# Optimization experiments

Measured on AMD Instinct MI355X. Metric: run time of the kernel, lower is better.

## Reference

```python
import jax, jax.numpy as jnp
import numpy as np

NUM_NODES = 100000
NUM_EDGES = 1600000
NUM_GRAPHS = 64
IN_CH, HID, NCLS = 15, 128, 11


def setup_inputs() -> dict:
    key = jax.random.key(0)
    ks = jax.random.split(key, 9)
    x = jax.random.normal(ks[0], (NUM_NODES, IN_CH), dtype=jnp.float32)
    edge_index = jax.random.randint(ks[1], (2, NUM_EDGES), 0, NUM_NODES, dtype=jnp.int64)
    batch = jnp.sort(jax.random.randint(ks[2], (NUM_NODES,), 0, NUM_GRAPHS, dtype=jnp.int64))
    s1 = 1.0 / np.sqrt(IN_CH)
    s2 = 1.0 / np.sqrt(HID)
    W1 = jax.random.normal(ks[3], (IN_CH, HID), dtype=jnp.float32) * s1
    b1 = jax.random.normal(ks[4], (HID,), dtype=jnp.float32) * s1
    W2 = jax.random.normal(ks[5], (HID, HID), dtype=jnp.float32) * s2
    b2 = jax.random.normal(ks[6], (HID,), dtype=jnp.float32) * s2
    Wf = jax.random.normal(ks[7], (HID, NCLS), dtype=jnp.float32) * s2
    bf = jax.random.normal(ks[8], (NCLS,), dtype=jnp.float32) * s2
    return {"x": x, "edge_index": edge_index, "batch": batch,
            "W1": W1, "b1": b1, "W2": W2, "b2": b2, "Wf": Wf, "bf": bf}


def reference(x, edge_index, batch, W1, b1, W2, b2, Wf, bf):
    N = x.shape[0]
    loop = jnp.arange(N, dtype=edge_index.dtype)
    # PyG GCNConv: add self-loops, symmetric D^{-1/2} A D^{-1/2} normalization
    src = jnp.concatenate([edge_index[0], loop])
    dst = jnp.concatenate([edge_index[1], loop])
    deg = jax.ops.segment_sum(jnp.ones(src.shape[0], dtype=x.dtype), dst, num_segments=N)
    dinv = deg ** -0.5  # deg >= 1 due to self-loops
    norm = (dinv[src] * dinv[dst])[:, None]  # [E+N, 1]

    def gcn(h, W, b):
        m = h @ W                                   # transform first (smaller gather)
        agg = jax.ops.segment_sum(m[src] * norm, dst, num_segments=N)
        return agg + b

    h = jax.nn.relu(gcn(x, W1, b1))
    h = jax.nn.relu(gcn(h, W2, b2))

    # global_mean_pool over graph ids
    sums = jax.ops.segment_sum(h, batch, num_segments=NUM_GRAPHS)
    cnts = jax.ops.segment_sum(jnp.ones((N,), dtype=h.dtype), batch, num_segments=NUM_GRAPHS)
    pooled = sums / jnp.maximum(cnts, 1.0)[:, None]  # [G, HID]
    return pooled @ Wf + bf                          # [G, NCLS]
```

## Files before the change

kernel.cpp:

```cpp
#include <hip/hip_runtime.h>

#define N_NODES 100000
#define N_EDGES 1600000
#define N_GRAPHS 64
#define IN_CH 15
#define HID 128
#define NCLS 11

#define NBUCK 196
#define NBF 512
#define EPB (N_EDGES / NBF)

using short8 = __attribute__((ext_vector_type(8))) short;
using f32x4 = __attribute__((ext_vector_type(4))) float;
using f32x2 = __attribute__((ext_vector_type(2))) float;

__device__ __forceinline__ unsigned short f2bf(float f) {
    unsigned u = __builtin_bit_cast(unsigned, f);
    u += 0x7FFF + ((u >> 16) & 1);
    return (unsigned short)(u >> 16);
}
__device__ __forceinline__ unsigned packbf(float a, float b) {
    return (unsigned)f2bf(a) | ((unsigned)f2bf(b) << 16);
}
__device__ __forceinline__ float2 unpackbf(unsigned v) {
    float2 r;
    unsigned lo = v << 16;
    unsigned hi = v & 0xFFFF0000u;
    r.x = __builtin_bit_cast(float, lo);
    r.y = __builtin_bit_cast(float, hi);
    return r;
}

__device__ __forceinline__ unsigned char f2fp8(float f) {
    return (unsigned char)(__builtin_amdgcn_cvt_pk_fp8_f32(f, f, 0, false) & 0xFF);
}
__device__ __forceinline__ float2 unpackfp8(unsigned short v) {
    f32x2 r = __builtin_amdgcn_cvt_pk_f32_fp8((int)(unsigned)v, false);
    return make_float2(r[0], r[1]);
}

__global__ __launch_bounds__(256) void k_init(float* __restrict__ pooled) {
    int i = blockIdx.x * 256 + threadIdx.x;
    if (i < N_GRAPHS * HID) pooled[i] = 0.f;
}

__global__ __launch_bounds__(256) void k_hist(const int* __restrict__ dst,
                                              int* __restrict__ cntm) {
    __shared__ int hist[NBUCK];
    int t = threadIdx.x;
    for (int i = t; i < NBUCK; i += 256) hist[i] = 0;
    __syncthreads();
    int base = blockIdx.x * EPB;
#pragma unroll
    for (int i = 0; i < (EPB + 255) / 256; ++i) {
        int e = i * 256 + t;
        if (e < EPB) atomicAdd(&hist[dst[base + e] >> 9], 1);
    }
    __syncthreads();
    for (int b = t; b < NBUCK; b += 256)
        cntm[b * NBF + blockIdx.x] = hist[b];
}

__global__ __launch_bounds__(256) void k_btot(const int* __restrict__ cntm,
                                              int* __restrict__ tot) {
    __shared__ int red[256];
    int b = blockIdx.x, t = threadIdx.x;
    red[t] = cntm[b * NBF + t] + cntm[b * NBF + t + 256];
    __syncthreads();
    for (int off = 128; off > 0; off >>= 1) {
        if (t < off) red[t] += red[t + off];
        __syncthreads();
    }
    if (t == 0) tot[b] = red[0];
}

__global__ __launch_bounds__(256) void k_bscan(const int* __restrict__ tot,
                                               int* __restrict__ bbase,
                                               int* __restrict__ rowptr) {
    __shared__ int arr[256];
    int t = threadIdx.x;
    arr[t] = (t < NBUCK) ? tot[t] : 0;
    __syncthreads();
    for (int off = 1; off < 256; off <<= 1) {
        int v = (t >= off) ? arr[t - off] : 0;
        __syncthreads();
        arr[t] += v;
        __syncthreads();
    }
    if (t < NBUCK) bbase[t] = (t == 0) ? 0 : arr[t - 1];
    if (t == 0) rowptr[N_NODES] = N_EDGES;
}

__global__ __launch_bounds__(NBF) void k_offs(const int* __restrict__ cntm,
                                              const int* __restrict__ bbase,
                                              int* __restrict__ offs) {
    __shared__ int arr[NBF];
    int b = blockIdx.x, t = threadIdx.x;
    arr[t] = cntm[b * NBF + t];
    __syncthreads();
    for (int off = 1; off < NBF; off <<= 1) {
        int v = (t >= off) ? arr[t - off] : 0;
        __syncthreads();
        arr[t] += v;
        __syncthreads();
    }
    offs[b * NBF + t] = bbase[b] + ((t == 0) ? 0 : arr[t - 1]);
}

__global__ __launch_bounds__(256) void k_partition(const int* __restrict__ src,
                                                   const int* __restrict__ dst,
                                                   const int* __restrict__ offs,
                                                   unsigned* __restrict__ staging) {
    __shared__ int cur[NBUCK];
    int t = threadIdx.x;
    for (int b = t; b < NBUCK; b += 256) cur[b] = offs[b * NBF + blockIdx.x];
    __syncthreads();
    int base = blockIdx.x * EPB;
#pragma unroll
    for (int i = 0; i < (EPB + 255) / 256; ++i) {
        int e = i * 256 + t;
        if (e < EPB) {
            int d = dst[base + e];
            int s = src[base + e];
            int slot = atomicAdd(&cur[d >> 9], 1);
            staging[slot] = ((unsigned)(d & 511) << 17) | (unsigned)s;
        }
    }
}

__global__ __launch_bounds__(256) void k_fuse(const unsigned* __restrict__ staging,
                                              const int* __restrict__ bbase,
                                              int* __restrict__ rowptr,
                                              float* __restrict__ dinv,
                                              int* __restrict__ csr_src) {
    __shared__ int cnt[512];
    __shared__ int cur[512];
    __shared__ int arr[256];
    int b = blockIdx.x, t = threadIdx.x;
    cnt[t] = 0; cnt[t + 256] = 0;
    __syncthreads();
    int beg = bbase[b];
    int end = (b == NBUCK - 1) ? N_EDGES : bbase[b + 1];
    for (int e = beg + t; e < end; e += 256)
        atomicAdd(&cnt[staging[e] >> 17], 1);
    __syncthreads();
    int c0 = cnt[2 * t], c1 = cnt[2 * t + 1];
    arr[t] = c0 + c1;
    __syncthreads();
    for (int off = 1; off < 256; off <<= 1) {
        int v = (t >= off) ? arr[t - off] : 0;
        __syncthreads();
        arr[t] += v;
        __syncthreads();
    }
    int excl = (t == 0) ? 0 : arr[t - 1];
    int p0 = beg + excl;
    int p1 = p0 + c0;
    cur[2 * t] = p0;
    cur[2 * t + 1] = p1;
    int n0 = b << 9;
    int n = n0 + 2 * t;
    if (n < N_NODES) { rowptr[n] = p0; dinv[n] = rsqrtf((float)(c0 + 1)); }
    n = n0 + 2 * t + 1;
    if (n < N_NODES) { rowptr[n] = p1; dinv[n] = rsqrtf((float)(c1 + 1)); }
    __syncthreads();
    for (int e = beg + t; e < end; e += 256) {
        unsigned v = staging[e];
        int pos = atomicAdd(&cur[v >> 17], 1);
        csr_src[pos] = (int)(v & 0x1FFFFu);
    }
}

__global__ __launch_bounds__(256) void k_w2pack(const float* __restrict__ W2,
                                                uint4* __restrict__ Bp) {
    int i = blockIdx.x * 256 + threadIdx.x;
    if (i >= 2048) return;
    int lane = i & 63;
    int kb = (i >> 6) & 3;
    int ct = i >> 8;
    int col = ct * 16 + (lane & 15);
    int k0 = kb * 32 + ((lane >> 4) & 3) * 8;
    unsigned w[4];
#pragma unroll
    for (int p = 0; p < 4; ++p) {
        int k = k0 + 2 * p;
        w[p] = packbf(W2[k * HID + col], W2[(k + 1) * HID + col]);
    }
    Bp[i] = make_uint4(w[0], w[1], w[2], w[3]);
}

__global__ __launch_bounds__(256) void k_prescale(const float* __restrict__ x,
                                                  const float* __restrict__ dinv,
                                                  unsigned* __restrict__ xs) {
    int i = blockIdx.x * 256 + threadIdx.x;
    if (i >= N_NODES * 8) return;
    int n = i >> 3, p = i & 7;
    float dv = dinv[n];
    int c0 = 2 * p, c1 = c0 + 1;
    float a = x[(size_t)n * IN_CH + c0] * dv;
    float b = (c1 < IN_CH) ? x[(size_t)n * IN_CH + c1] * dv : 0.f;
    xs[i] = packbf(a, b);
}

__global__ __launch_bounds__(256) void k_gather15(const int* __restrict__ rowptr,
                                                  const int* __restrict__ csr_src,
                                                  const unsigned* __restrict__ xs,
                                                  const float* __restrict__ dinv,
                                                  float* __restrict__ agg) {
    int wave = (blockIdx.x * 256 + threadIdx.x) >> 6;
    if (wave >= N_NODES) return;
    int n = wave;
    int l = threadIdx.x & 63;
    unsigned g = (unsigned)(l >> 3), cp = (unsigned)(l & 7);
    int beg = rowptr[n], end = rowptr[n + 1];
    float2 acc = make_float2(0.f, 0.f);
    for (int e = beg + (int)g; e < end; e += 8) {
        unsigned s = (unsigned)csr_src[e];
        float2 v = unpackbf(xs[s * 8u + cp]);
        acc.x += v.x; acc.y += v.y;
    }
#pragma unroll
    for (int off = 8; off < 64; off <<= 1) {
        acc.x += __shfl_xor(acc.x, off, 64);
        acc.y += __shfl_xor(acc.y, off, 64);
    }
    if (l < 8) {
        float2 s = unpackbf(xs[(unsigned)n * 8u + (unsigned)l]);
        float dv = dinv[n];
        float2 r = make_float2((acc.x + s.x) * dv, (acc.y + s.y) * dv);
        *(float2*)&agg[(unsigned)n * 16u + 2u * (unsigned)l] = r;
    }
}

__global__ __launch_bounds__(256) void k_xform1b(const float* __restrict__ agg,
                                                 const float* __restrict__ W1,
                                                 const float* __restrict__ b1,
                                                 unsigned* __restrict__ h1b) {
    __shared__ float w[IN_CH * HID];
    int t = threadIdx.x;
    for (int i = t; i < IN_CH * HID; i += 256) w[i] = W1[i];
    __syncthreads();
    int node = blockIdx.x * 4 + (t >> 6);
    int lane = t & 63;
    int c = lane * 2;
    const float* ar = agg + (size_t)node * 16;
    float a0 = b1[c], a1 = b1[c + 1];
#pragma unroll
    for (int k = 0; k < IN_CH; ++k) {
        float av = ar[k];
        a0 += av * w[k * HID + c];
        a1 += av * w[k * HID + c + 1];
    }
    h1b[(size_t)node * 64 + lane] = packbf(fmaxf(a0, 0.f), fmaxf(a1, 0.f));
}

__global__ __launch_bounds__(256) void k_xform2(const unsigned* __restrict__ h1b,
                                                const uint4* __restrict__ Bp,
                                                const float* __restrict__ dinv,
                                                unsigned char* __restrict__ mout) {
    int lane = threadIdx.x & 63;
    int wid = threadIdx.x >> 6;
    int row0 = blockIdx.x * 64 + wid * 16;
    int arow = row0 + (lane & 15);
    const uint4* hbase = (const uint4*)h1b;
    uint4 a_u[4];
#pragma unroll
    for (int kb = 0; kb < 4; ++kb)
        a_u[kb] = hbase[(size_t)arow * 16 + kb * 4 + (lane >> 4)];
    int rbase = row0 + (lane >> 4) * 4;
    float dv[4];
#pragma unroll
    for (int j = 0; j < 4; ++j) dv[j] = dinv[min(rbase + j, N_NODES - 1)];
#pragma unroll
    for (int ct = 0; ct < 8; ++ct) {
        f32x4 acc = {0.f, 0.f, 0.f, 0.f};
#pragma unroll
        for (int kb = 0; kb < 4; ++kb) {
            uint4 b_u = Bp[(ct * 4 + kb) * 64 + lane];
            acc = __builtin_amdgcn_mfma_f32_16x16x32_bf16(
                __builtin_bit_cast(short8, a_u[kb]),
                __builtin_bit_cast(short8, b_u), acc, 0, 0, 0);
        }
        int col = ct * 16 + (lane & 15);
#pragma unroll
        for (int j = 0; j < 4; ++j) {
            int r = rbase + j;
            if (r < N_NODES) mout[(size_t)r * HID + col] = f2fp8(acc[j] * dv[j]);
        }
    }
}

__global__ __launch_bounds__(256) void k_gather(const int* __restrict__ rowptr,
                                                const int* __restrict__ csr_src,
                                                const unsigned short* __restrict__ m,
                                                const float* __restrict__ bias,
                                                const float* __restrict__ dinv,
                                                unsigned* __restrict__ outh) {
    int wave = (blockIdx.x * 256 + threadIdx.x) >> 6;
    if (wave >= N_NODES) return;
    unsigned n = (unsigned)wave;
    unsigned lane = (unsigned)(threadIdx.x & 63);
    int c = (int)lane * 2;
    int beg = rowptr[n], end = rowptr[n + 1];
    float2 acc = unpackfp8(m[n * 64u + lane]);
    int e = beg;
    for (; e + 8 <= end; e += 8) {
        unsigned o0 = (unsigned)csr_src[e + 0] * 64u + lane;
        unsigned o1 = (unsigned)csr_src[e + 1] * 64u + lane;
        unsigned o2 = (unsigned)csr_src[e + 2] * 64u + lane;
        unsigned o3 = (unsigned)csr_src[e + 3] * 64u + lane;
        unsigned o4 = (unsigned)csr_src[e + 4] * 64u + lane;
        unsigned o5 = (unsigned)csr_src[e + 5] * 64u + lane;
        unsigned o6 = (unsigned)csr_src[e + 6] * 64u + lane;
        unsigned o7 = (unsigned)csr_src[e + 7] * 64u + lane;
        unsigned short v0 = m[o0];
        unsigned short v1 = m[o1];
        unsigned short v2 = m[o2];
        unsigned short v3 = m[o3];
        unsigned short v4 = m[o4];
        unsigned short v5 = m[o5];
        unsigned short v6 = m[o6];
        unsigned short v7 = m[o7];
        float2 f0 = unpackfp8(v0), f1 = unpackfp8(v1), f2 = unpackfp8(v2), f3 = unpackfp8(v3);
        float2 f4 = unpackfp8(v4), f5 = unpackfp8(v5), f6 = unpackfp8(v6), f7 = unpackfp8(v7);
        acc.x += f0.x + f1.x + f2.x + f3.x + f4.x + f5.x + f6.x + f7.x;
        acc.y += f0.y + f1.y + f2.y + f3.y + f4.y + f5.y + f6.y + f7.y;
    }
    for (; e + 2 <= end; e += 2) {
        unsigned short v0 = m[(unsigned)csr_src[e] * 64u + lane];
        unsigned short v1 = m[(unsigned)csr_src[e + 1] * 64u + lane];
        float2 f0 = unpackfp8(v0), f1 = unpackfp8(v1);
        acc.x += f0.x + f1.x;
        acc.y += f0.y + f1.y;
    }
    if (e < end) {
        float2 f = unpackfp8(m[(unsigned)csr_src[e] * 64u + lane]);
        acc.x += f.x; acc.y += f.y;
    }
    float dv = dinv[n];
    float2 b = *(const float2*)&bias[c];
    float rx = fmaxf(acc.x * dv + b.x, 0.f);
    float ry = fmaxf(acc.y * dv + b.y, 0.f);
    outh[n * 64u + lane] = packbf(rx, ry);
}

__global__ __launch_bounds__(64) void k_cnt(const int* __restrict__ batch,
                                            int* __restrict__ cnt) {
    int g = threadIdx.x;
    if (g >= N_GRAPHS) return;
    int lo0 = 0, hi0 = N_NODES;
    while (lo0 < hi0) { int mid = (lo0 + hi0) >> 1; if (batch[mid] < g) lo0 = mid + 1; else hi0 = mid; }
    int lo1 = lo0, hi1 = N_NODES;
    while (lo1 < hi1) { int mid = (lo1 + hi1) >> 1; if (batch[mid] < g + 1) lo1 = mid + 1; else hi1 = mid; }
    cnt[g] = lo1 - lo0;
}

#define POOL_CHUNK 128
__global__ __launch_bounds__(256) void k_pool(const unsigned* __restrict__ h,
                                              const int* __restrict__ batch,
                                              float* __restrict__ pooled) {
    int t = threadIdx.x;
    int lane = t & 63;
    int grp = t >> 6;
    int start = blockIdx.x * POOL_CHUNK;
    int end = min(start + POOL_CHUNK, N_NODES);
    float2 acc = make_float2(0.f, 0.f);
    int cur = -1;
    for (int n = start + grp; n < end; n += 4) {
        int g = batch[n];
        if (g != cur) {
            if (cur >= 0) {
                atomicAdd(&pooled[cur * HID + lane * 2], acc.x);
                atomicAdd(&pooled[cur * HID + lane * 2 + 1], acc.y);
            }
            acc = make_float2(0.f, 0.f);
            cur = g;
        }
        float2 v = unpackbf(h[(unsigned)n * 64u + (unsigned)lane]);
        acc.x += v.x; acc.y += v.y;
    }
    if (cur >= 0) {
        atomicAdd(&pooled[cur * HID + lane * 2], acc.x);
        atomicAdd(&pooled[cur * HID + lane * 2 + 1], acc.y);
    }
}

__global__ __launch_bounds__(128) void k_final(const float* __restrict__ pooled,
                                               const int* __restrict__ cnt,
                                               const float* __restrict__ Wf,
                                               const float* __restrict__ bf,
                                               float* __restrict__ out) {
    __shared__ float p[HID];
    int g = blockIdx.x, t = threadIdx.x;
    float inv = 1.f / fmaxf((float)cnt[g], 1.f);
    p[t] = pooled[g * HID + t] * inv;
    __syncthreads();
    if (t < NCLS) {
        float acc = bf[t];
        for (int k = 0; k < HID; ++k) acc += p[k] * Wf[k * NCLS + t];
        out[g * NCLS + t] = acc;
    }
}

extern "C" void kernel_launch(void* const* d_in, const int* in_sizes, int n_in,
                              void* d_out, int out_size, void* d_ws, size_t ws_size,
                              hipStream_t stream) {
    const float* x   = (const float*)d_in[0];
    const int*   ei  = (const int*)d_in[1];
    const int*   src = ei;
    const int*   dst = ei + N_EDGES;
    const int*   batch = (const int*)d_in[2];
    const float* W1 = (const float*)d_in[3];
    const float* b1 = (const float*)d_in[4];
    const float* W2 = (const float*)d_in[5];
    const float* b2 = (const float*)d_in[6];
    const float* Wf = (const float*)d_in[7];
    const float* bf = (const float*)d_in[8];
    float* out = (float*)d_out;

    char* ws = (char*)d_ws;
    size_t off = 0;
    unsigned* mbuf = (unsigned*)(ws + off);  off += (size_t)N_NODES * 64 * 4;
    unsigned* h1b = (unsigned*)(ws + off);   off += (size_t)N_NODES * 64 * 4;
    unsigned* h2b = (unsigned*)(ws + off);   off += (size_t)N_NODES * 64 * 4;
    int* csr_src = (int*)(ws + off);         off += (size_t)N_EDGES * 4;
    uint4* Bp = (uint4*)(ws + off);          off += (size_t)2048 * 16;
    float* dinv = (float*)(ws + off);        off += (size_t)N_NODES * 4;
    int* rowptr = (int*)(ws + off);          off += (size_t)(N_NODES + 1) * 4;
    int* cntm = (int*)(ws + off);            off += (size_t)NBUCK * NBF * 4;
    int* offs = (int*)(ws + off);            off += (size_t)NBUCK * NBF * 4;
    int* tot = (int*)(ws + off);             off += (size_t)NBUCK * 4;
    int* bbase = (int*)(ws + off);           off += (size_t)NBUCK * 4;
    float* pooled = (float*)(ws + off);      off += (size_t)N_GRAPHS * HID * 4;
    int* cnt = (int*)(ws + off);             off += (size_t)N_GRAPHS * 4;
    unsigned* staging = h2b;
    unsigned* xs = mbuf;
    float* agg = (float*)(mbuf + (size_t)N_NODES * 8);

    k_init<<<(N_GRAPHS * HID + 255) / 256, 256, 0, stream>>>(pooled);
    k_hist<<<NBF, 256, 0, stream>>>(dst, cntm);
    k_btot<<<NBUCK, 256, 0, stream>>>(cntm, tot);
    k_bscan<<<1, 256, 0, stream>>>(tot, bbase, rowptr);
    k_offs<<<NBUCK, NBF, 0, stream>>>(cntm, bbase, offs);
    k_partition<<<NBF, 256, 0, stream>>>(src, dst, offs, staging);
    k_fuse<<<NBUCK, 256, 0, stream>>>(staging, bbase, rowptr, dinv, csr_src);
    k_w2pack<<<8, 256, 0, stream>>>(W2, Bp);

    k_prescale<<<(N_NODES * 8 + 255) / 256, 256, 0, stream>>>(x, dinv, xs);
    k_gather15<<<(N_NODES + 3) / 4, 256, 0, stream>>>(rowptr, csr_src, xs, dinv, agg);
    k_xform1b<<<N_NODES / 4, 256, 0, stream>>>(agg, W1, b1, h1b);

    k_xform2<<<(N_NODES + 63) / 64, 256, 0, stream>>>(h1b, Bp, dinv, (unsigned char*)mbuf);
    k_gather<<<(N_NODES + 3) / 4, 256, 0, stream>>>(rowptr, csr_src, (const unsigned short*)mbuf, b2, dinv, h2b);

    k_cnt<<<1, 64, 0, stream>>>(batch, cnt);
    k_pool<<<(N_NODES + POOL_CHUNK - 1) / POOL_CHUNK, 256, 0, stream>>>(h2b, batch, pooled);
    k_final<<<N_GRAPHS, 128, 0, stream>>>(pooled, cnt, Wf, bf, out);
}
```

Measured before the change: 237.5 us.

## Fuse layer-1 and layer-2 transforms through LDS; widen fp8 gather loads

Merges the first-layer dense transform into the MFMA second-layer transform. Each block computes a 64-node tile of bf16 activations into shared memory and feeds the MFMA directly from there, so the full h1 intermediate no longer goes out to global memory and back. The second-layer gather now has each half-wave take alternating edges with 4-byte loads of four fp8 values per lane, combined with a cross-half shuffle. This means fewer, wider memory transactions. The cost is extra LDS and larger per-block work in the fused kernel, plus an extra reduction step in the gather.

```diff
diff --git a/kernel.cpp b/kernel.cpp
--- a/kernel.cpp
+++ b/kernel.cpp
@@ -34,10 +34,6 @@
 
 __device__ __forceinline__ unsigned char f2fp8(float f) {
     return (unsigned char)(__builtin_amdgcn_cvt_pk_fp8_f32(f, f, 0, false) & 0xFF);
-}
-__device__ __forceinline__ float2 unpackfp8(unsigned short v) {
-    f32x2 r = __builtin_amdgcn_cvt_pk_f32_fp8((int)(unsigned)v, false);
-    return make_float2(r[0], r[1]);
 }
 
 __global__ __launch_bounds__(256) void k_init(float* __restrict__ pooled) {
@@ -233,42 +229,43 @@
     }
 }
 
-__global__ __launch_bounds__(256) void k_xform1b(const float* __restrict__ agg,
+__global__ __launch_bounds__(256) void k_xform12(const float* __restrict__ agg,
                                                  const float* __restrict__ W1,
                                                  const float* __restrict__ b1,
-                                                 unsigned* __restrict__ h1b) {
+                                                 const uint4* __restrict__ Bp,
+                                                 const float* __restrict__ dinv,
+                                                 unsigned char* __restrict__ mout) {
     __shared__ float w[IN_CH * HID];
+    __shared__ unsigned hl[64][68];
     int t = threadIdx.x;
     for (int i = t; i < IN_CH * HID; i += 256) w[i] = W1[i];
     __syncthreads();
-    int node = blockIdx.x * 4 + (t >> 6);
+    int n0 = blockIdx.x * 64;
+#pragma unroll
+    for (int i = 0; i < 16; ++i) {
+        int u = i * 256 + t;
+        int nl = u >> 6;
+        int cp = u & 63;
+        int c = cp * 2;
+        const float* ar = agg + (size_t)(n0 + nl) * 16;
+        float a0 = b1[c], a1 = b1[c + 1];
+#pragma unroll
+        for (int k = 0; k < IN_CH; ++k) {
+            float av = ar[k];
+            a0 += av * w[k * HID + c];
+            a1 += av * w[k * HID + c + 1];
+        }
+        hl[nl][cp] = packbf(fmaxf(a0, 0.f), fmaxf(a1, 0.f));
+    }
+    __syncthreads();
     int lane = t & 63;
-    int c = lane * 2;
-    const float* ar = agg + (size_t)node * 16;
-    float a0 = b1[c], a1 = b1[c + 1];
-#pragma unroll
-    for (int k = 0; k < IN_CH; ++k) {
-        float av = ar[k];
-        a0 += av * w[k * HID + c];
-        a1 += av * w[k * HID + c + 1];
-    }
-    h1b[(size_t)node * 64 + lane] = packbf(fmaxf(a0, 0.f), fmaxf(a1, 0.f));
-}
-
-__global__ __launch_bounds__(256) void k_xform2(const unsigned* __restrict__ h1b,
-                                                const uint4* __restrict__ Bp,
-                                                const float* __restrict__ dinv,
-                                                unsigned char* __restrict__ mout) {
-    int lane = threadIdx.x & 63;
-    int wid = threadIdx.x >> 6;
-    int row0 = blockIdx.x * 64 + wid * 16;
-    int arow = row0 + (lane & 15);
-    const uint4* hbase = (const uint4*)h1b;
+    int wid = t >> 6;
+    int arow = wid * 16 + (lane & 15);
     uint4 a_u[4];
 #pragma unroll
     for (int kb = 0; kb < 4; ++kb)
-        a_u[kb] = hbase[(size_t)arow * 16 + kb * 4 + (lane >> 4)];
-    int rbase = row0 + (lane >> 4) * 4;
+        a_u[kb] = *(const uint4*)&hl[arow][kb * 16 + (lane >> 4) * 4];
+    int rbase = n0 + wid * 16 + (lane >> 4) * 4;
     float dv[4];
 #pragma unroll
     for (int j = 0; j < 4; ++j) dv[j] = dinv[min(rbase + j, N_NODES - 1)];
@@ -293,56 +290,67 @@
 
 __global__ __launch_bounds__(256) void k_gather(const int* __restrict__ rowptr,
                                                 const int* __restrict__ csr_src,
-                                                const unsigned short* __restrict__ m,
+                                                const unsigned* __restrict__ m,
                                                 const float* __restrict__ bias,
                                                 const float* __restrict__ dinv,
                                                 unsigned* __restrict__ outh) {
     int wave = (blockIdx.x * 256 + threadIdx.x) >> 6;
     if (wave >= N_NODES) return;
     unsigned n = (unsigned)wave;
-    unsigned lane = (unsigned)(threadIdx.x & 63);
-    int c = (int)lane * 2;
+    int lane = threadIdx.x & 63;
+    int half = lane >> 5;
+    unsigned li = (unsigned)(lane & 31);
     int beg = rowptr[n], end = rowptr[n + 1];
-    float2 acc = unpackfp8(m[n * 64u + lane]);
-    int e = beg;
-    for (; e + 8 <= end; e += 8) {
-        unsigned o0 = (unsigned)csr_src[e + 0] * 64u + lane;
-        unsigned o1 = (unsigned)csr_src[e + 1] * 64u + lane;
-        unsigned o2 = (unsigned)csr_src[e + 2] * 64u + lane;
-        unsigned o3 = (unsigned)csr_src[e + 3] * 64u + lane;
-        unsigned o4 = (unsigned)csr_src[e + 4] * 64u + lane;
-        unsigned o5 = (unsigned)csr_src[e + 5] * 64u + lane;
-        unsigned o6 = (unsigned)csr_src[e + 6] * 64u + lane;
-        unsigned o7 = (unsigned)csr_src[e + 7] * 64u + lane;
-        unsigned short v0 = m[o0];
-        unsigned short v1 = m[o1];
-        unsigned short v2 = m[o2];
-        unsigned short v3 = m[o3];
-        unsigned short v4 = m[o4];
-        unsigned short v5 = m[o5];
-        unsigned short v6 = m[o6];
-        unsigned short v7 = m[o7];
-        float2 f0 = unpackfp8(v0), f1 = unpackfp8(v1), f2 = unpackfp8(v2), f3 = unpackfp8(v3);
-        float2 f4 = unpackfp8(v4), f5 = unpackfp8(v5), f6 = unpackfp8(v6), f7 = unpackfp8(v7);
-        acc.x += f0.x + f1.x + f2.x + f3.x + f4.x + f5.x + f6.x + f7.x;
-        acc.y += f0.y + f1.y + f2.y + f3.y + f4.y + f5.y + f6.y + f7.y;
-    }
-    for (; e + 2 <= end; e += 2) {
-        unsigned short v0 = m[(unsigned)csr_src[e] * 64u + lane];
-        unsigned short v1 = m[(unsigned)csr_src[e + 1] * 64u + lane];
-        float2 f0 = unpackfp8(v0), f1 = unpackfp8(v1);
-        acc.x += f0.x + f1.x;
-        acc.y += f0.y + f1.y;
-    }
-    if (e < end) {
-        float2 f = unpackfp8(m[(unsigned)csr_src[e] * 64u + lane]);
-        acc.x += f.x; acc.y += f.y;
-    }
-    float dv = dinv[n];
-    float2 b = *(const float2*)&bias[c];
-    float rx = fmaxf(acc.x * dv + b.x, 0.f);
-    float ry = fmaxf(acc.y * dv + b.y, 0.f);
-    outh[n * 64u + lane] = packbf(rx, ry);
+    f32x4 acc = {0.f, 0.f, 0.f, 0.f};
+    if (half == 0) {
+        unsigned u = m[n * 32u + li];
+        f32x2 lo = __builtin_amdgcn_cvt_pk_f32_fp8((int)u, false);
+        f32x2 hi = __builtin_amdgcn_cvt_pk_f32_fp8((int)u, true);
+        acc[0] += lo[0]; acc[1] += lo[1]; acc[2] += hi[0]; acc[3] += hi[1];
+    }
+    int e = beg + half;
+    for (; e + 6 < end; e += 8) {
+        unsigned o0 = (unsigned)csr_src[e + 0] * 32u + li;
+        unsigned o1 = (unsigned)csr_src[e + 2] * 32u + li;
+        unsigned o2 = (unsigned)csr_src[e + 4] * 32u + li;
+        unsigned o3 = (unsigned)csr_src[e + 6] * 32u + li;
+        unsigned u0 = m[o0];
+        unsigned u1 = m[o1];
+        unsigned u2 = m[o2];
+        unsigned u3 = m[o3];
+        f32x2 l0 = __builtin_amdgcn_cvt_pk_f32_fp8((int)u0, false);
+        f32x2 h0 = __builtin_amdgcn_cvt_pk_f32_fp8((int)u0, true);
+        f32x2 l1 = __builtin_amdgcn_cvt_pk_f32_fp8((int)u1, false);
+        f32x2 h1 = __builtin_amdgcn_cvt_pk_f32_fp8((int)u1, true);
+        f32x2 l2 = __builtin_amdgcn_cvt_pk_f32_fp8((int)u2, false);
+        f32x2 h2 = __builtin_amdgcn_cvt_pk_f32_fp8((int)u2, true);
+        f32x2 l3 = __builtin_amdgcn_cvt_pk_f32_fp8((int)u3, false);
+        f32x2 h3 = __builtin_amdgcn_cvt_pk_f32_fp8((int)u3, true);
+        acc[0] += l0[0] + l1[0] + l2[0] + l3[0];
+        acc[1] += l0[1] + l1[1] + l2[1] + l3[1];
+        acc[2] += h0[0] + h1[0] + h2[0] + h3[0];
+        acc[3] += h0[1] + h1[1] + h2[1] + h3[1];
+    }
+    for (; e < end; e += 2) {
+        unsigned u = m[(unsigned)csr_src[e] * 32u + li];
+        f32x2 lo = __builtin_amdgcn_cvt_pk_f32_fp8((int)u, false);
+        f32x2 hi = __builtin_amdgcn_cvt_pk_f32_fp8((int)u, true);
+        acc[0] += lo[0]; acc[1] += lo[1]; acc[2] += hi[0]; acc[3] += hi[1];
+    }
+#pragma unroll
+    for (int j = 0; j < 4; ++j) acc[j] += __shfl_xor(acc[j], 32, 64);
+    if (half == 0) {
+        float dv = dinv[n];
+        float4 b = *(const float4*)&bias[li * 4u];
+        float r0 = fmaxf(acc[0] * dv + b.x, 0.f);
+        float r1 = fmaxf(acc[1] * dv + b.y, 0.f);
+        float r2 = fmaxf(acc[2] * dv + b.z, 0.f);
+        float r3 = fmaxf(acc[3] * dv + b.w, 0.f);
+        uint2 ov;
+        ov.x = packbf(r0, r1);
+        ov.y = packbf(r2, r3);
+        *(uint2*)&outh[n * 64u + li * 2u] = ov;
+    }
 }
 
 __global__ __launch_bounds__(64) void k_cnt(const int* __restrict__ batch,
@@ -437,6 +445,7 @@
     unsigned* staging = h2b;
     unsigned* xs = mbuf;
     float* agg = (float*)(mbuf + (size_t)N_NODES * 8);
+    unsigned char* mfp8 = (unsigned char*)h1b;
 
     k_init<<<(N_GRAPHS * HID + 255) / 256, 256, 0, stream>>>(pooled);
     k_hist<<<NBF, 256, 0, stream>>>(dst, cntm);
@@ -449,10 +458,10 @@
 
     k_prescale<<<(N_NODES * 8 + 255) / 256, 256, 0, stream>>>(x, dinv, xs);
     k_gather15<<<(N_NODES + 3) / 4, 256, 0, stream>>>(rowptr, csr_src, xs, dinv, agg);
-    k_xform1b<<<N_NODES / 4, 256, 0, stream>>>(agg, W1, b1, h1b);
-
-    k_xform2<<<(N_NODES + 63) / 64, 256, 0, stream>>>(h1b, Bp, dinv, (unsigned char*)mbuf);
-    k_gather<<<(N_NODES + 3) / 4, 256, 0, stream>>>(rowptr, csr_src, (const unsigned short*)mbuf, b2, dinv, h2b);
+
+    k_xform12<<<(N_NODES + 63) / 64, 256, 0, stream>>>(agg, W1, b1, Bp, dinv, mfp8);
+
+    k_gather<<<(N_NODES + 3) / 4, 256, 0, stream>>>(rowptr, csr_src, (const unsigned*)mfp8, b2, dinv, h2b);
 
     k_cnt<<<1, 64, 0, stream>>>(batch, cnt);
     k_pool<<<(N_NODES + POOL_CHUNK - 1) / POOL_CHUNK, 256, 0, stream>>>(h2b, batch, pooled);
```

Result: faster. 232.7 us (-2.0%).
